# Performance work log

Hardware: AMD Instinct MI355X
Metric: run time of the kernel (lower is better)

## Reference

```python
import jax, jax.numpy as jnp
import numpy as np

B, T, D = 4, 2048, 1024
E = 16            # routed experts
S = 2             # shared experts
MOE_TOPK = 2
COSINE_LAMBDA = 0.1


def setup_inputs() -> dict:
    key = jax.random.key(0)
    k_x, k_g, k_sh, k_rt = jax.random.split(key, 4)
    x = jax.random.normal(k_x, (B, T, D), dtype=jnp.float32)
    gate_w = jax.random.normal(k_g, (E, D), dtype=jnp.float32) * 0.02
    gate_b = jnp.zeros((E,), dtype=jnp.float32)
    shared_experts = jax.random.normal(k_sh, (S, D), dtype=jnp.float32) * 0.1
    routed_experts = jax.random.normal(k_rt, (E, D), dtype=jnp.float32) * 0.1
    return {"x": x, "gate_w": gate_w, "gate_b": gate_b,
            "shared_experts": shared_experts, "routed_experts": routed_experts}


def reference(x, gate_w, gate_b, shared_experts, routed_experts):
    b, t, d = x.shape
    n = b * t
    hidden = x.reshape(n, d)                                   # [N, D]

    # ---- router ----
    logits = hidden @ gate_w.T + gate_b                        # [N, E]
    probs = jax.nn.softmax(logits, axis=-1)                    # stable (shift-invariant)
    topk_vals, topk_idx = jax.lax.top_k(probs, MOE_TOPK)       # [N, K]
    if MOE_TOPK == 1:
        weights = jnp.ones_like(topk_vals)
    else:
        weights = topk_vals / jnp.clip(topk_vals.sum(-1, keepdims=True), 1e-6)

    # ---- shared experts (always active): sum_e hidden * w_e ----
    shared_sum = hidden * shared_experts.sum(0)                # [N, D]

    # ---- dense all-expert elementwise scale (as in original) ----
    routed_outs = hidden[None, :, :] * routed_experts[:, None, :]   # [E, N, D]

    # ---- diversity loss: cosine sim between flattened expert outputs ----
    flat = routed_outs.reshape(E, -1)                          # [E, N*D]
    norms = jnp.maximum(jnp.linalg.norm(flat, axis=1, keepdims=True), 1e-8)
    normed = flat / norms
    sim = jnp.clip(normed @ normed.T, -1.0, 1.0)               # [E, E]
    mask = 1.0 - jnp.eye(E, dtype=sim.dtype)
    div_loss = (sim * mask).sum() / max(E * (E - 1), 1) * COSINE_LAMBDA

    # ---- top-k gather + weighted combine ----
    routed_nd = routed_outs.transpose(1, 0, 2)                 # [N, E, D]
    sel = jnp.take_along_axis(routed_nd, topk_idx[:, :, None], axis=1)  # [N, K, D]
    dyn_sum = (sel * weights[:, :, None]).sum(axis=1)          # [N, D]

    out = (shared_sum + dyn_sum).reshape(b, t, d)
    return out, div_loss
```

## Files before the change

### kernel.cpp

```cpp
#include <hip/hip_runtime.h>

#define NTOK 8192
#define DDIM 1024
#define NEXP 16
#define NPAIR 136
#define XROW 1032
#define NBLK 1024
#define NGRP 64

#define WS_GWT  0
#define WS_SLOT 16384
#define WS_FIN  (WS_SLOT + NBLK * DDIM)
#define WS_CNT  (WS_FIN + DDIM)

__global__ __launch_bounds__(256) void moe_prep(
    const float* __restrict__ gate_w,
    float* __restrict__ ws)
{
    const int gid = blockIdx.x * 256 + threadIdx.x;
    const int e = gid & 15;
    const int d4 = gid >> 4;
    const float4* gw4 = (const float4*)gate_w;
    float4* gwT4 = (float4*)(ws + WS_GWT);
    gwT4[d4 * 16 + e] = gw4[e * 256 + d4];
    if (gid < DDIM) (ws + WS_FIN)[gid] = 0.f;
    if (gid < NGRP + 1) ((int*)ws)[WS_CNT + gid] = 0;
}

__global__ __launch_bounds__(256, 4) void moe_fused(
    const float* __restrict__ x,
    const float* __restrict__ gate_b,
    const float* __restrict__ sh,
    const float* __restrict__ re,
    float* __restrict__ out,
    float* __restrict__ ws)
{
    __shared__ __align__(16) float xt[8][XROW];
    __shared__ float nr[NEXP];
    __shared__ float lsum;
    __shared__ int   role;

    const int t = threadIdx.x;
    const int b = blockIdx.x;
    const float4* gwT4 = (const float4*)(ws + WS_GWT);
    int* cnt = (int*)ws + WS_CNT;

    float4 ss = make_float4(0.f, 0.f, 0.f, 0.f);
    {
        const float4* x4 = (const float4*)x + (size_t)b * 2048;
        #pragma unroll
        for (int i = 0; i < 8; ++i) {
            float4 v = x4[i * 256 + t];
            *(float4*)&xt[i][4 * t] = v;
            ss.x = fmaf(v.x, v.x, ss.x);
            ss.y = fmaf(v.y, v.y, ss.y);
            ss.z = fmaf(v.z, v.z, ss.z);
            ss.w = fmaf(v.w, v.w, ss.w);
        }
    }
    __syncthreads();

    const int lane = t & 63;
    const int wave = t >> 6;
    const int e = lane & 15;
    const int h = (lane >> 4) & 1;
    const int g = lane >> 5;

    const int tokL = wave * 2 + g;
    const float* xrow = &xt[tokL][h * 512];
    const float4* gt = gwT4 + h * 128 * 16;
    float4 a4 = make_float4(0.f, 0.f, 0.f, 0.f);
    #pragma unroll 8
    for (int i = 0; i < 128; ++i) {
        float4 xv = *(const float4*)(xrow + 4 * i);
        float4 gv = gt[i * 16 + e];
        a4.x = fmaf(xv.x, gv.x, a4.x);
        a4.y = fmaf(xv.y, gv.y, a4.y);
        a4.z = fmaf(xv.z, gv.z, a4.z);
        a4.w = fmaf(xv.w, gv.w, a4.w);
    }
    float acc = (a4.x + a4.y) + (a4.z + a4.w);
    acc += __shfl_xor(acc, 16, 64);
    acc += gate_b[e];

    float v0 = -3.0e38f, v1 = -3.0e38f;
    int i0 = 0, i1 = 0;
    const int base = lane & 32;
    #pragma unroll
    for (int j = 0; j < NEXP; ++j) {
        float lv = __shfl(acc, base + j, 64);
        if (lv > v0)      { v1 = v0; i1 = i0; v0 = lv; i0 = j; }
        else if (lv > v1) { v1 = lv; i1 = j; }
    }
    float ex = __expf(v1 - v0);
    float w0 = 1.f / (1.f + ex);
    float w1 = ex * w0;

    float4 shs[4];
    {
        const float4* s0 = (const float4*)sh;
        const float4* s1 = (const float4*)(sh + DDIM);
        #pragma unroll
        for (int j = 0; j < 4; ++j) {
            float4 p = s0[lane + 64 * j];
            float4 q = s1[lane + 64 * j];
            shs[j] = make_float4(p.x + q.x, p.y + q.y, p.z + q.z, p.w + q.w);
        }
    }

    #pragma unroll
    for (int tk = 0; tk < 2; ++tk) {
        const int src = tk << 5;
        float a0 = __shfl(w0, src, 64);
        float a1 = __shfl(w1, src, 64);
        int   e0 = __shfl(i0, src, 64);
        int   e1 = __shfl(i1, src, 64);
        const int tokL2 = wave * 2 + tk;
        const float4* xr = (const float4*)&xt[tokL2][0];
        const float4* r0 = (const float4*)(re + (size_t)e0 * DDIM);
        const float4* r1 = (const float4*)(re + (size_t)e1 * DDIM);
        float4* o = (float4*)(out + ((size_t)b * 8 + tokL2) * DDIM);
        #pragma unroll
        for (int j = 0; j < 4; ++j) {
            float4 xv = xr[lane + 64 * j];
            float4 b0 = r0[lane + 64 * j];
            float4 b1 = r1[lane + 64 * j];
            float4 r;
            r.x = xv.x * (shs[j].x + a0 * b0.x + a1 * b1.x);
            r.y = xv.y * (shs[j].y + a0 * b0.y + a1 * b1.y);
            r.z = xv.z * (shs[j].z + a0 * b0.z + a1 * b1.z);
            r.w = xv.w * (shs[j].w + a0 * b0.w + a1 * b1.w);
            o[lane + 64 * j] = r;
        }
    }

    {
        float* slot = ws + WS_SLOT + (size_t)b * DDIM;
        __hip_atomic_store(&slot[4 * t + 0], ss.x, __ATOMIC_RELAXED, __HIP_MEMORY_SCOPE_AGENT);
        __hip_atomic_store(&slot[4 * t + 1], ss.y, __ATOMIC_RELAXED, __HIP_MEMORY_SCOPE_AGENT);
        __hip_atomic_store(&slot[4 * t + 2], ss.z, __ATOMIC_RELAXED, __HIP_MEMORY_SCOPE_AGENT);
        __hip_atomic_store(&slot[4 * t + 3], ss.w, __ATOMIC_RELAXED, __HIP_MEMORY_SCOPE_AGENT);
    }
    __syncthreads();
    if (t == 0) {
        int a = atomicAdd(&cnt[b & (NGRP - 1)], 1);
        role = (a == 15);
    }
    __syncthreads();
    if (!role) return;

    __builtin_amdgcn_fence(__ATOMIC_ACQUIRE, "agent");
    const int grp = b & (NGRP - 1);
    float4 racc;
    {
        const float4* sl4 = (const float4*)(ws + WS_SLOT) + (size_t)grp * 256 + t;
        racc = sl4[0];
        #pragma unroll
        for (int k = 1; k < 16; ++k) {
            float4 v = sl4[(size_t)k * 16384];
            racc.x += v.x; racc.y += v.y; racc.z += v.z; racc.w += v.w;
        }
    }
    {
        float* s_fin = ws + WS_FIN;
        atomicAdd(&s_fin[4 * t + 0], racc.x);
        atomicAdd(&s_fin[4 * t + 1], racc.y);
        atomicAdd(&s_fin[4 * t + 2], racc.z);
        atomicAdd(&s_fin[4 * t + 3], racc.w);
    }
    __syncthreads();
    if (t == 0) {
        int f = atomicAdd(&cnt[NGRP], 1);
        role = (f == NGRP - 1);
    }
    __syncthreads();
    if (!role) return;

    __builtin_amdgcn_fence(__ATOMIC_ACQUIRE, "agent");
    float* smem = &xt[0][0];
    {
        const float4* sf4 = (const float4*)(ws + WS_FIN);
        ((float4*)smem)[t] = sf4[t];
    }
    if (t == 0) lsum = 0.f;
    __syncthreads();

    float gacc = 0.f;
    int pe = 0, pf = 0;
    if (t < NPAIR) {
        int rem = t;
        while (rem >= NEXP - pe) { rem -= NEXP - pe; ++pe; }
        pf = pe + rem;
        const float4* ra = (const float4*)(re + (size_t)pe * DDIM);
        const float4* rb = (const float4*)(re + (size_t)pf * DDIM);
        const float4* sl = (const float4*)smem;
        #pragma unroll 4
        for (int i = 0; i < 256; ++i) {
            float4 s = sl[i];
            float4 u = ra[i];
            float4 v = rb[i];
            gacc = fmaf(s.x * u.x, v.x, gacc);
            gacc = fmaf(s.y * u.y, v.y, gacc);
            gacc = fmaf(s.z * u.z, v.z, gacc);
            gacc = fmaf(s.w * u.w, v.w, gacc);
        }
        if (pe == pf) nr[pe] = fmaxf(sqrtf(gacc), 1e-8f);
    }
    __syncthreads();
    if (t < NPAIR && pe != pf) {
        float sim = gacc / (nr[pe] * nr[pf]);
        sim = fminf(1.f, fmaxf(-1.f, sim));
        atomicAdd(&lsum, 2.f * sim);
    }
    __syncthreads();
    if (t == 0)
        out[(size_t)NTOK * DDIM] = lsum / (float)(NEXP * (NEXP - 1)) * 0.1f;
}

extern "C" void kernel_launch(void* const* d_in, const int* in_sizes, int n_in,
                              void* d_out, int out_size, void* d_ws, size_t ws_size,
                              hipStream_t stream) {
    const float* x  = (const float*)d_in[0];
    const float* gw = (const float*)d_in[1];
    const float* gb = (const float*)d_in[2];
    const float* sh = (const float*)d_in[3];
    const float* re = (const float*)d_in[4];
    float* out = (float*)d_out;
    float* ws = (float*)d_ws;

    moe_prep<<<16, 256, 0, stream>>>(gw, ws);
    moe_fused<<<NBLK, 256, 0, stream>>>(x, gb, sh, re, out, ws);
}
```

Measured before the change: 145.0 us.

## Distribute Gram-matrix computation across group-finisher blocks instead of final block

Blocks now form contiguous groups of 16, and the last block in each group sums its group's sum-of-squares slots. It then computes the 136 pairwise expert Gram partials over that group's slice and atomically adds them into a small global Gram buffer. The single final block then only reads 136 accumulated values to form norms and cosine similarities. This removes the serialized 1024-wide atomic reduction and the 256-iteration Gram loop from the critical tail of the last block. In exchange, 64 blocks each run a Gram loop and issue 136 float atomics.

```diff
diff --git a/kernel.cpp b/kernel.cpp
--- a/kernel.cpp
+++ b/kernel.cpp
@@ -7,11 +7,12 @@
 #define XROW 1032
 #define NBLK 1024
 #define NGRP 64
+#define GSZ  16
 
 #define WS_GWT  0
 #define WS_SLOT 16384
-#define WS_FIN  (WS_SLOT + NBLK * DDIM)
-#define WS_CNT  (WS_FIN + DDIM)
+#define WS_G    (WS_SLOT + NBLK * DDIM)
+#define WS_CNT  (WS_G + 256)
 
 __global__ __launch_bounds__(256) void moe_prep(
     const float* __restrict__ gate_w,
@@ -23,7 +24,7 @@
     const float4* gw4 = (const float4*)gate_w;
     float4* gwT4 = (float4*)(ws + WS_GWT);
     gwT4[d4 * 16 + e] = gw4[e * 256 + d4];
-    if (gid < DDIM) (ws + WS_FIN)[gid] = 0.f;
+    if (gid < 256) (ws + WS_G)[gid] = 0.f;
     if (gid < NGRP + 1) ((int*)ws)[WS_CNT + gid] = 0;
 }
 
@@ -143,46 +144,24 @@
     }
     __syncthreads();
     if (t == 0) {
-        int a = atomicAdd(&cnt[b & (NGRP - 1)], 1);
-        role = (a == 15);
+        int a = atomicAdd(&cnt[b >> 4], 1);
+        role = (a == GSZ - 1);
     }
     __syncthreads();
     if (!role) return;
 
     __builtin_amdgcn_fence(__ATOMIC_ACQUIRE, "agent");
-    const int grp = b & (NGRP - 1);
-    float4 racc;
-    {
-        const float4* sl4 = (const float4*)(ws + WS_SLOT) + (size_t)grp * 256 + t;
-        racc = sl4[0];
-        #pragma unroll
-        for (int k = 1; k < 16; ++k) {
-            float4 v = sl4[(size_t)k * 16384];
+    const int grp = b >> 4;
+    {
+        const float4* sl4 = (const float4*)(ws + WS_SLOT) + (size_t)grp * (GSZ * 256) + t;
+        float4 racc = sl4[0];
+        #pragma unroll
+        for (int k = 1; k < GSZ; ++k) {
+            float4 v = sl4[k * 256];
             racc.x += v.x; racc.y += v.y; racc.z += v.z; racc.w += v.w;
         }
-    }
-    {
-        float* s_fin = ws + WS_FIN;
-        atomicAdd(&s_fin[4 * t + 0], racc.x);
-        atomicAdd(&s_fin[4 * t + 1], racc.y);
-        atomicAdd(&s_fin[4 * t + 2], racc.z);
-        atomicAdd(&s_fin[4 * t + 3], racc.w);
-    }
-    __syncthreads();
-    if (t == 0) {
-        int f = atomicAdd(&cnt[NGRP], 1);
-        role = (f == NGRP - 1);
-    }
-    __syncthreads();
-    if (!role) return;
-
-    __builtin_amdgcn_fence(__ATOMIC_ACQUIRE, "agent");
-    float* smem = &xt[0][0];
-    {
-        const float4* sf4 = (const float4*)(ws + WS_FIN);
-        ((float4*)smem)[t] = sf4[t];
-    }
-    if (t == 0) lsum = 0.f;
+        *(float4*)&xt[0][4 * t] = racc;
+    }
     __syncthreads();
 
     float gacc = 0.f;
@@ -193,8 +172,8 @@
         pf = pe + rem;
         const float4* ra = (const float4*)(re + (size_t)pe * DDIM);
         const float4* rb = (const float4*)(re + (size_t)pf * DDIM);
-        const float4* sl = (const float4*)smem;
-        #pragma unroll 4
+        const float4* sl = (const float4*)&xt[0][0];
+        #pragma unroll 8
         for (int i = 0; i < 256; ++i) {
             float4 s = sl[i];
             float4 u = ra[i];
@@ -204,11 +183,27 @@
             gacc = fmaf(s.z * u.z, v.z, gacc);
             gacc = fmaf(s.w * u.w, v.w, gacc);
         }
-        if (pe == pf) nr[pe] = fmaxf(sqrtf(gacc), 1e-8f);
+        atomicAdd(ws + WS_G + t, gacc);
+    }
+    __syncthreads();
+    if (t == 0) {
+        int f = atomicAdd(&cnt[NGRP], 1);
+        role = (f == NGRP - 1);
+    }
+    __syncthreads();
+    if (!role) return;
+
+    __builtin_amdgcn_fence(__ATOMIC_ACQUIRE, "agent");
+    float gv = 0.f;
+    if (t < NPAIR) gv = (ws + WS_G)[t];
+    if (t == 0) lsum = 0.f;
+    if (t < NEXP) {
+        int idx = t * NEXP - (t * (t - 1)) / 2;
+        nr[t] = fmaxf(sqrtf((ws + WS_G)[idx]), 1e-8f);
     }
     __syncthreads();
     if (t < NPAIR && pe != pf) {
-        float sim = gacc / (nr[pe] * nr[pf]);
+        float sim = gv / (nr[pe] * nr[pf]);
         sim = fminf(1.f, fmaxf(-1.f, sim));
         atomicAdd(&lsum, 2.f * sim);
     }
```

Measured after the change: 208.3 us. 43.7% more time.
